# Optimization experiments

Measured on AMD Instinct MI355X. Metric: run time of the kernel, lower is better.

The kernel has to match this reference:

```python
import jax, jax.numpy as jnp
import numpy as np

N = 50000      # nodes
E = 800000     # edges (avg degree 16)
B = 8          # graphs in batch
H = 128        # hidden (message_passer out_channels)
FF = 64        # fourier_feat_dim -> fourier features have dim 2*FF
REPEATS = 4    # repeats_training
OUT = 4        # output_dim
IN_X = 5
IN_MASK = 3

def _fourier(x, M):
    # https://arxiv.org/pdf/2106.02795.pdf : [cos(xM), sin(xM)] / sqrt(2F)
    p = x @ M
    return jnp.concatenate([jnp.cos(p), jnp.sin(p)], axis=-1) / jnp.sqrt(2.0 * M.shape[1])

def _seg_mean(v, idx, n):
    s = jax.ops.segment_sum(v, idx, num_segments=n)
    c = jax.ops.segment_sum(jnp.ones((v.shape[0],), v.dtype), idx, num_segments=n)
    return s / jnp.maximum(c, 1.0)[:, None]

def setup_inputs() -> dict:
    key = jax.random.key(0)
    ks = jax.random.split(key, 16)
    x = jax.random.normal(ks[0], (N, IN_X), jnp.float32)
    x_mask = jax.random.bernoulli(ks[1], 0.1, (N, IN_MASK)).astype(jnp.float32)
    edge_index = jax.random.randint(ks[2], (2, E), 0, N)
    edge_attr = jax.random.normal(ks[3], (E, 3), jnp.float32)
    pos = jax.random.uniform(ks[4], (N, 2), jnp.float32)
    batch = jnp.sort(jax.random.randint(ks[5], (N,), 0, B))
    sampling_points = jax.random.uniform(ks[6], (2,), jnp.float32)
    fourier_mat = jax.random.normal(ks[7], (2, FF), jnp.float32)  # learnable, init N(0,1)
    W_enc = jax.random.normal(ks[8], (IN_X + IN_MASK, H), jnp.float32) * 0.1
    b_enc = jnp.zeros((H,), jnp.float32)
    W_msg = jax.random.normal(ks[9], (2 * H + 3, H), jnp.float32) * 0.05
    b_msg = jnp.zeros((H,), jnp.float32)
    W_upd = jax.random.normal(ks[10], (4 * H, H), jnp.float32) * 0.05
    b_upd = jnp.zeros((H,), jnp.float32)
    W_dec = jax.random.normal(ks[11], (H, OUT), jnp.float32) * 0.1
    b_dec = jnp.zeros((OUT,), jnp.float32)
    return dict(x=x, x_mask=x_mask, edge_index=edge_index, edge_attr=edge_attr,
                pos=pos, batch=batch, sampling_points=sampling_points,
                fourier_mat=fourier_mat, W_enc=W_enc, b_enc=b_enc,
                W_msg=W_msg, b_msg=b_msg, W_upd=W_upd, b_upd=b_upd,
                W_dec=W_dec, b_dec=b_dec)

def reference(x, x_mask, edge_index, edge_attr, pos, batch, sampling_points,
              fourier_mat, W_enc, b_enc, W_msg, b_msg, W_upd, b_upd, W_dec, b_dec):
    bc = x_mask[:, -1]                                   # 0/1 BC flag
    x_full = jnp.concatenate([x, x_mask], axis=1)        # x = concat([x, x_mask])
    keys_ff = _fourier(pos, fourier_mat)                 # input fourier features [N, 2F]
    h = jax.nn.relu(x_full @ W_enc + b_enc)              # encoder -> [N, H]

    # x_BC: scatter-mean over BC nodes per graph (computed once)
    bc_sum = jax.ops.segment_sum(h * bc[:, None], batch, num_segments=B)
    bc_cnt = jax.ops.segment_sum(bc, batch, num_segments=B)
    x_BC = bc_sum / jnp.maximum(bc_cnt, 1.0)[:, None]    # [B, H]

    x_graph = _seg_mean(h, batch, B)                     # global_mean_pool [B, H]
    src, dst = edge_index[0], edge_index[1]
    deg = jnp.maximum(jax.ops.segment_sum(jnp.ones((E,), h.dtype), dst, num_segments=N), 1.0)

    for _ in range(REPEATS):  # repeated message passing
        m = jax.nn.relu(jnp.concatenate([h[src], h[dst], edge_attr], axis=1) @ W_msg + b_msg)
        agg = jax.ops.segment_sum(m, dst, num_segments=N) / deg[:, None]  # scatter-mean
        upd_in = jnp.concatenate([h, agg, x_graph[batch], x_BC[batch]], axis=1)
        h = h + jax.nn.relu(upd_in @ W_upd + b_upd)
        x_graph = _seg_mean(h, batch, B)                 # re-pool each repeat

    decoded = h @ W_dec + b_dec                          # [N, OUT]

    # kernelized fourier-feature interpolation at the sampling point
    q = _fourier(sampling_points, fourier_mat)           # [2F]
    nq = q / jnp.linalg.norm(q)
    nk = keys_ff / jnp.linalg.norm(keys_ff, axis=1, keepdims=True)
    vals_sum = h.sum(axis=0)                             # [H]
    kwv = nk.T @ h                                       # [2F, H]
    ks_sum = nk.sum(axis=0)                              # [2F]
    enc = (vals_sum + nq @ kwv) / (N + nq @ ks_sum)      # [H]
    U_sampled = enc @ W_dec + b_dec                      # [OUT]
    # pack (U_sampled, decoded) into one array: row 0 = sampled point, rows 1: = nodes
    return jnp.concatenate([U_sampled[None, :], decoded], axis=0)
```

## Files before the change

kernel.cpp:

```cpp
#include <hip/hip_runtime.h>
#include <math.h>

#define Nn 50000
#define Ee 800000
#define Bb 8
#define ROUNDS 4
#define KWVB 512
#define SCB 196
#define AP 40
#define HP 132
#define KS 40
#define NBK 196
#define P1B 391
#define CHUNK 2047

typedef __attribute__((ext_vector_type(8))) short bf16x8;
typedef __attribute__((ext_vector_type(4))) float f32x4;

__device__ inline short f2bf(float f) {
  union { float f; unsigned u; } v; v.f = f;
  unsigned r = v.u + 0x7fff + ((v.u >> 16) & 1);
  return (short)(r >> 16);
}
__device__ inline float bf2f(short s) {
  union { float f; unsigned u; } v; v.u = ((unsigned)(unsigned short)s) << 16;
  return v.f;
}

__global__ __launch_bounds__(256) void encode_seg(
    const float* __restrict__ x, const float* __restrict__ xm,
    const int* __restrict__ batch, const float* __restrict__ W,
    const float* __restrict__ b, float* __restrict__ h,
    float* __restrict__ gsum, float* __restrict__ gcnt,
    float* __restrict__ bcsum, float* __restrict__ bccnt) {
  __shared__ float xs5[128 * 5];
  __shared__ float xm3[128 * 3];
  __shared__ float ls[Bb * 128];
  __shared__ float lb[Bb * 128];
  __shared__ float lc[Bb], lbc[Bb];
  const int t = threadIdx.x;
  const int nBase = blockIdx.x * 128;
  const int j = t & 127, half = t >> 7;
  const int base5 = nBase * 5, base3 = nBase * 3;
  for (int q = t; q < 640; q += 256) xs5[q] = (base5 + q < Nn * 5) ? x[base5 + q] : 0.f;
  for (int q = t; q < 384; q += 256) xm3[q] = (base3 + q < Nn * 3) ? xm[base3 + q] : 0.f;
  for (int q = t; q < Bb * 128; q += 256) { ls[q] = 0.f; lb[q] = 0.f; }
  if (t < Bb) { lc[t] = 0.f; lbc[t] = 0.f; }
  float Wcol[8];
#pragma unroll
  for (int k = 0; k < 8; k++) Wcol[k] = W[k * 128 + j];
  const float bj = b[j];
  __syncthreads();
  int curb = -1;
  float runh = 0.f, runb = 0.f, runc = 0.f, runbc = 0.f;
  for (int kk = 0; kk < 64; kk++) {
    int i = nBase + kk * 2 + half;
    if (i >= Nn) break;
    int li = i - nBase;
    float acc = bj;
#pragma unroll
    for (int k = 0; k < 5; k++) acc = fmaf(xs5[li * 5 + k], Wcol[k], acc);
#pragma unroll
    for (int k = 0; k < 3; k++) acc = fmaf(xm3[li * 3 + k], Wcol[5 + k], acc);
    float v = fmaxf(acc, 0.f);
    h[(size_t)i * 128 + j] = v;
    float bc = xm3[li * 3 + 2];
    int g = batch[i];
    if (g != curb) {
      if (curb >= 0) {
        atomicAdd(&ls[curb * 128 + j], runh);
        atomicAdd(&lb[curb * 128 + j], runb);
        if (j == 0) { atomicAdd(&lc[curb], runc); atomicAdd(&lbc[curb], runbc); }
      }
      curb = g; runh = runb = runc = runbc = 0.f;
    }
    runh += v; runb += v * bc;
    if (j == 0) { runc += 1.f; runbc += bc; }
  }
  if (curb >= 0) {
    atomicAdd(&ls[curb * 128 + j], runh);
    atomicAdd(&lb[curb * 128 + j], runb);
    if (j == 0) { atomicAdd(&lc[curb], runc); atomicAdd(&lbc[curb], runbc); }
  }
  __syncthreads();
  for (int q = t; q < Bb * 128; q += 256) {
    float a = ls[q], c = lb[q];
    if (a != 0.f) atomicAdd(&gsum[q], a);
    if (c != 0.f) atomicAdd(&bcsum[q], c);
  }
  if (t < Bb) { atomicAdd(&gcnt[t], lc[t]); atomicAdd(&bccnt[t], lbc[t]); }
}

__global__ __launch_bounds__(256) void split_w_kernel(
    const float* __restrict__ Wm, const float* __restrict__ Wu,
    short* __restrict__ Wmt_h, short* __restrict__ Wmt_l,
    short* __restrict__ Wut_h, short* __restrict__ Wut_l) {
  int idx = blockIdx.x * 256 + threadIdx.x;
  if (idx < 32768) {
    int k = idx & 127, n = (idx >> 7) & 127, y = idx >> 14;
    float w = Wm[(size_t)(y * 128 + k) * 128 + n];
    short hi = f2bf(w);
    Wmt_h[idx] = hi;
    Wmt_l[idx] = f2bf(w - bf2f(hi));
  } else if (idx < 65536) {
    int j = idx - 32768;
    int k = j & 255, n = j >> 8;
    float w = Wu[(size_t)k * 128 + n];
    short hi = f2bf(w);
    Wut_h[j] = hi;
    Wut_l[j] = f2bf(w - bf2f(hi));
  }
}

__global__ __launch_bounds__(256) void bkt_cnt(const int* __restrict__ ei,
                                               int* __restrict__ bktcnt) {
  __shared__ int hist[NBK];
  int t = threadIdx.x;
  for (int q = t; q < NBK; q += 256) hist[q] = 0;
  __syncthreads();
  int base = blockIdx.x * CHUNK;
  int end = base + CHUNK < Ee ? base + CHUNK : Ee;
  for (int e = base + t; e < end; e += 256) atomicAdd(&hist[ei[Ee + e] >> 8], 1);
  __syncthreads();
  for (int q = t; q < NBK; q += 256)
    if (hist[q]) atomicAdd(&bktcnt[q], hist[q]);
}
__global__ __launch_bounds__(256) void bkt_scan(const int* __restrict__ bktcnt,
                                                int* __restrict__ bktbase,
                                                int* __restrict__ bktcur) {
  __shared__ int s[256];
  int t = threadIdx.x;
  int v = (t < NBK) ? bktcnt[t] : 0;
  s[t] = v;
  __syncthreads();
  for (int off = 1; off < 256; off <<= 1) {
    int x = (t >= off) ? s[t - off] : 0;
    __syncthreads();
    s[t] += x;
    __syncthreads();
  }
  int ex = s[t] - v;
  if (t < NBK) { bktbase[t] = ex; bktcur[t] = ex; }
  if (t == NBK - 1) bktbase[NBK] = ex + v;
}
__global__ __launch_bounds__(256) void bkt_part(
    const int* __restrict__ ei, const float* __restrict__ ea,
    int* __restrict__ bktcur, int2* __restrict__ recA,
    unsigned char* __restrict__ dlo) {
  __shared__ int hist[NBK], lbase[NBK], lcur[NBK];
  int t = threadIdx.x;
  for (int q = t; q < NBK; q += 256) hist[q] = 0;
  __syncthreads();
  int base = blockIdx.x * CHUNK;
  int end = base + CHUNK < Ee ? base + CHUNK : Ee;
  for (int e = base + t; e < end; e += 256) atomicAdd(&hist[ei[Ee + e] >> 8], 1);
  __syncthreads();
  for (int q = t; q < NBK; q += 256) {
    int c = hist[q];
    lbase[q] = c ? atomicAdd(&bktcur[q], c) : 0;
    lcur[q] = 0;
  }
  __syncthreads();
  for (int e = base + t; e < end; e += 256) {
    int d = ei[Ee + e];
    int bk = d >> 8;
    int p = lbase[bk] + atomicAdd(&lcur[bk], 1);
    unsigned r0 = (unsigned)ei[e] |
                  ((unsigned)(unsigned short)f2bf(ea[3 * (size_t)e + 0]) << 16);
    unsigned r1 = (unsigned)(unsigned short)f2bf(ea[3 * (size_t)e + 1]) |
                  ((unsigned)(unsigned short)f2bf(ea[3 * (size_t)e + 2]) << 16);
    recA[p] = make_int2((int)r0, (int)r1);
    dlo[p] = (unsigned char)(d & 255);
  }
}
__global__ __launch_bounds__(256) void dst_cnt(const int* __restrict__ bktbase,
                                               const unsigned char* __restrict__ dlo,
                                               int* __restrict__ cnt) {
  __shared__ int hh[256];
  int t = threadIdx.x;
  hh[t] = 0;
  __syncthreads();
  int b = blockIdx.x;
  int lo = bktbase[b], hi = bktbase[b + 1];
  for (int i = lo + t; i < hi; i += 256) atomicAdd(&hh[dlo[i]], 1);
  __syncthreads();
  int d = b * 256 + t;
  if (d < Nn) cnt[d] = hh[t];
}
__global__ __launch_bounds__(256) void bsum_kernel(const int* __restrict__ cnt,
                                                   int* __restrict__ bsum) {
  __shared__ int wsum[4];
  int t = threadIdx.x;
  int i = blockIdx.x * 256 + t;
  int v = (i < Nn) ? cnt[i] : 0;
#pragma unroll
  for (int off = 32; off > 0; off >>= 1) v += __shfl_down(v, off);
  if ((t & 63) == 0) wsum[t >> 6] = v;
  __syncthreads();
  if (t == 0) bsum[blockIdx.x] = wsum[0] + wsum[1] + wsum[2] + wsum[3];
}
__global__ __launch_bounds__(256) void scan_top_kernel(const int* __restrict__ bsum,
                                                       int* __restrict__ boff) {
  __shared__ int s[256];
  int t = threadIdx.x;
  int v = (t < SCB) ? bsum[t] : 0;
  s[t] = v;
  __syncthreads();
  for (int off = 1; off < 256; off <<= 1) {
    int x = (t >= off) ? s[t - off] : 0;
    __syncthreads();
    s[t] += x;
    __syncthreads();
  }
  boff[t] = s[t] - v;
}
__global__ __launch_bounds__(256) void apply_kernel(
    const int* __restrict__ cnt, const int* __restrict__ boff,
    int* __restrict__ rowptr, float* __restrict__ invdeg) {
  __shared__ int s[256];
  int t = threadIdx.x;
  int i = blockIdx.x * 256 + t;
  int v = (i < Nn) ? cnt[i] : 0;
  s[t] = v;
  __syncthreads();
  for (int off = 1; off < 256; off <<= 1) {
    int x = (t >= off) ? s[t - off] : 0;
    __syncthreads();
    s[t] += x;
    __syncthreads();
  }
  int ex = boff[blockIdx.x] + s[t] - v;
  if (i < Nn) {
    rowptr[i] = ex;
    invdeg[i] = 1.0f / fmaxf((float)v, 1.0f);
    if (i == Nn - 1) rowptr[Nn] = ex + v;
  }
}
__global__ __launch_bounds__(256) void bkt_fin(
    const int* __restrict__ bktbase, const int2* __restrict__ recA,
    const unsigned char* __restrict__ dlo, const int* __restrict__ rowptr,
    int2* __restrict__ rec) {
  __shared__ int cur[256];
  int t = threadIdx.x;
  int b = blockIdx.x;
  int d = b * 256 + t;
  cur[t] = (d < Nn) ? rowptr[d] : 0;
  __syncthreads();
  int lo = bktbase[b], hi = bktbase[b + 1];
  for (int i = lo + t; i < hi; i += 256) {
    int dl = dlo[i];
    int p = atomicAdd(&cur[dl], 1);
    rec[p] = recA[i];
  }
}

__global__ __launch_bounds__(128) void gb_static_kernel(
    const float* __restrict__ bcsum, const float* __restrict__ bccnt,
    const float* __restrict__ Wu, const float* __restrict__ bu,
    float* __restrict__ gbst) {
  __shared__ float xb[128];
  int g = blockIdx.x, t = threadIdx.x;
  xb[t] = bcsum[g * 128 + t] / fmaxf(bccnt[g], 1.f);
  __syncthreads();
  float acc = bu[t];
#pragma unroll 4
  for (int k = 0; k < 128; k++) acc = fmaf(xb[k], Wu[(size_t)(384 + k) * 128 + t], acc);
  gbst[g * 128 + t] = acc;
}

__global__ __launch_bounds__(128) void gb_dyn_kernel(
    const float* __restrict__ gsum, const float* __restrict__ gcnt,
    const float* __restrict__ gbst, const float* __restrict__ Wu,
    float* __restrict__ gb) {
  __shared__ float xg[128];
  int g = blockIdx.x, t = threadIdx.x;
  xg[t] = gsum[g * 128 + t] / fmaxf(gcnt[g], 1.f);
  __syncthreads();
  float acc = gbst[g * 128 + t];
#pragma unroll 4
  for (int k = 0; k < 128; k++) acc = fmaf(xg[k], Wu[(size_t)(256 + k) * 128 + t], acc);
  gb[g * 128 + t] = acc;
}

__global__ __launch_bounds__(256) void proj_mfma(
    const float* __restrict__ h, const short* __restrict__ Wth,
    unsigned char* __restrict__ hs8, unsigned short* __restrict__ hdbf) {
  __shared__ short Ah_s[128 * AP];
  __shared__ short Bh_s[128 * AP];
  const int t = threadIdx.x;
  const int nBase = blockIdx.x * 128;
  const int yoff = blockIdx.y * 16384;
  const int wave = t >> 6, lane = t & 63;
  const int ml = lane & 15, quad = lane >> 4;
  const int ko = quad * 8;

  f32x4 acc[2][8];
#pragma unroll
  for (int nt = 0; nt < 2; nt++)
#pragma unroll
    for (int mt = 0; mt < 8; mt++)
#pragma unroll
      for (int q = 0; q < 4; q++) acc[nt][mt][q] = 0.f;

  const int srow = t >> 1;
  const int kc = (t & 1) * 16;
  const int nd0 = nBase + srow;
  const int nn = nd0 < Nn ? nd0 : Nn - 1;

  for (int c = 0; c < 4; c++) {
    const float* p = &h[(size_t)nn * 128 + c * 32 + kc];
    float4 u0 = *(const float4*)(p + 0);
    float4 u1 = *(const float4*)(p + 4);
    float4 u2 = *(const float4*)(p + 8);
    float4 u3 = *(const float4*)(p + 12);
    const int k0 = c * 32;
    const bf16x8 gb0 = *(const bf16x8*)&Wth[(size_t)yoff + srow * 128 + k0 + kc];
    const bf16x8 gb1 = *(const bf16x8*)&Wth[(size_t)yoff + srow * 128 + k0 + kc + 8];
    float xs[16] = {u0.x,u0.y,u0.z,u0.w, u1.x,u1.y,u1.z,u1.w,
                    u2.x,u2.y,u2.z,u2.w, u3.x,u3.y,u3.z,u3.w};
    bf16x8 vh0, vh1;
#pragma unroll
    for (int j = 0; j < 8; j++) vh0[j] = f2bf(xs[j]);
#pragma unroll
    for (int j = 0; j < 8; j++) vh1[j] = f2bf(xs[8 + j]);
    __syncthreads();
    *(bf16x8*)&Ah_s[srow * AP + kc] = vh0;
    *(bf16x8*)&Ah_s[srow * AP + kc + 8] = vh1;
    *(bf16x8*)&Bh_s[srow * AP + kc] = gb0;
    *(bf16x8*)&Bh_s[srow * AP + kc + 8] = gb1;
    __syncthreads();
#pragma unroll
    for (int mt = 0; mt < 8; mt++) {
      const int ar = (mt * 16 + ml) * AP + ko;
      bf16x8 ah = *(const bf16x8*)&Ah_s[ar];
#pragma unroll
      for (int nt = 0; nt < 2; nt++) {
        const int br = (wave * 32 + nt * 16 + ml) * AP + ko;
        bf16x8 bh = *(const bf16x8*)&Bh_s[br];
        acc[nt][mt] = __builtin_amdgcn_mfma_f32_16x16x32_bf16(ah, bh, acc[nt][mt], 0, 0, 0);
      }
    }
  }
  if (blockIdx.y == 0) {
#pragma unroll
    for (int nt = 0; nt < 2; nt++) {
      const int ch = wave * 32 + nt * 16 + ml;
#pragma unroll
      for (int mt = 0; mt < 8; mt++) {
#pragma unroll
        for (int q = 0; q < 4; q++) {
          int nd = nBase + mt * 16 + quad * 4 + q;
          if (nd < Nn) {
            int pk = __builtin_amdgcn_cvt_pk_fp8_f32(acc[nt][mt][q], acc[nt][mt][q], 0, false);
            hs8[(size_t)nd * 128 + ch] = (unsigned char)(pk & 0xff);
          }
        }
      }
    }
  } else {
#pragma unroll
    for (int nt = 0; nt < 2; nt++) {
      const int ch = wave * 32 + nt * 16 + ml;
#pragma unroll
      for (int mt = 0; mt < 8; mt++) {
#pragma unroll
        for (int q = 0; q < 4; q++) {
          int nd = nBase + mt * 16 + quad * 4 + q;
          if (nd < Nn) hdbf[(size_t)nd * 128 + ch] = (unsigned short)f2bf(acc[nt][mt][q]);
        }
      }
    }
  }
}

__global__ __launch_bounds__(256) void agg_kernel(
    const unsigned char* __restrict__ hs8, const unsigned short* __restrict__ hdbf,
    unsigned short* __restrict__ aggbf, const int2* __restrict__ rec,
    const int* __restrict__ rowptr, const float* __restrict__ invdeg,
    const float* __restrict__ Wm, const float* __restrict__ bm) {
  int t = threadIdx.x;
  int hw = t >> 5, lane = t & 31;
  int v = blockIdx.x * 8 + hw;
  if (v >= Nn) return;
  int c0 = lane * 4;
  const float4 We0 = *(const float4*)&Wm[(size_t)256 * 128 + c0];
  const float4 We1 = *(const float4*)&Wm[(size_t)257 * 128 + c0];
  const float4 We2 = *(const float4*)&Wm[(size_t)258 * 128 + c0];
  const float4 b4  = *(const float4*)&bm[c0];
  const ushort4 hd4 = *(const ushort4*)&hdbf[(size_t)v * 128 + c0];
  const float bx = b4.x + bf2f((short)hd4.x), by = b4.y + bf2f((short)hd4.y),
              bz = b4.z + bf2f((short)hd4.z), bw = b4.w + bf2f((short)hd4.w);
  float ax = 0.f, ay = 0.f, az = 0.f, aw = 0.f;
  float ax2 = 0.f, ay2 = 0.f, az2 = 0.f, aw2 = 0.f;
  const int r0 = rowptr[v], r1 = rowptr[v + 1];
  int e = r0;
  for (; e + 2 <= r1; e += 2) {
    int2 q0 = rec[e], q1 = rec[e + 1];
    int s0 = q0.x & 0xffff, s1 = q1.x & 0xffff;
    unsigned hr0 = *(const unsigned*)&hs8[(size_t)s0 * 128 + c0];
    unsigned hr1 = *(const unsigned*)&hs8[(size_t)s1 * 128 + c0];
    float e00 = bf2f((short)(q0.x >> 16));
    float e01 = bf2f((short)(q0.y & 0xffff));
    float e02 = bf2f((short)(q0.y >> 16));
    float e10 = bf2f((short)(q1.x >> 16));
    float e11 = bf2f((short)(q1.y & 0xffff));
    float e12 = bf2f((short)(q1.y >> 16));
    float h0x = __builtin_amdgcn_cvt_f32_fp8(hr0, 0);
    float h0y = __builtin_amdgcn_cvt_f32_fp8(hr0, 1);
    float h0z = __builtin_amdgcn_cvt_f32_fp8(hr0, 2);
    float h0w = __builtin_amdgcn_cvt_f32_fp8(hr0, 3);
    float h1x = __builtin_amdgcn_cvt_f32_fp8(hr1, 0);
    float h1y = __builtin_amdgcn_cvt_f32_fp8(hr1, 1);
    float h1z = __builtin_amdgcn_cvt_f32_fp8(hr1, 2);
    float h1w = __builtin_amdgcn_cvt_f32_fp8(hr1, 3);
    ax += fmaxf(fmaf(e00, We0.x, fmaf(e01, We1.x, fmaf(e02, We2.x, h0x + bx))), 0.f);
    ay += fmaxf(fmaf(e00, We0.y, fmaf(e01, We1.y, fmaf(e02, We2.y, h0y + by))), 0.f);
    az += fmaxf(fmaf(e00, We0.z, fmaf(e01, We1.z, fmaf(e02, We2.z, h0z + bz))), 0.f);
    aw += fmaxf(fmaf(e00, We0.w, fmaf(e01, We1.w, fmaf(e02, We2.w, h0w + bw))), 0.f);
    ax2 += fmaxf(fmaf(e10, We0.x, fmaf(e11, We1.x, fmaf(e12, We2.x, h1x + bx))), 0.f);
    ay2 += fmaxf(fmaf(e10, We0.y, fmaf(e11, We1.y, fmaf(e12, We2.y, h1y + by))), 0.f);
    az2 += fmaxf(fmaf(e10, We0.z, fmaf(e11, We1.z, fmaf(e12, We2.z, h1z + bz))), 0.f);
    aw2 += fmaxf(fmaf(e10, We0.w, fmaf(e11, We1.w, fmaf(e12, We2.w, h1w + bw))), 0.f);
  }
  if (e < r1) {
    int2 q0 = rec[e];
    int s0 = q0.x & 0xffff;
    unsigned hr0 = *(const unsigned*)&hs8[(size_t)s0 * 128 + c0];
    float e00 = bf2f((short)(q0.x >> 16));
    float e01 = bf2f((short)(q0.y & 0xffff));
    float e02 = bf2f((short)(q0.y >> 16));
    float h0x = __builtin_amdgcn_cvt_f32_fp8(hr0, 0);
    float h0y = __builtin_amdgcn_cvt_f32_fp8(hr0, 1);
    float h0z = __builtin_amdgcn_cvt_f32_fp8(hr0, 2);
    float h0w = __builtin_amdgcn_cvt_f32_fp8(hr0, 3);
    ax += fmaxf(fmaf(e00, We0.x, fmaf(e01, We1.x, fmaf(e02, We2.x, h0x + bx))), 0.f);
    ay += fmaxf(fmaf(e00, We0.y, fmaf(e01, We1.y, fmaf(e02, We2.y, h0y + by))), 0.f);
    az += fmaxf(fmaf(e00, We0.z, fmaf(e01, We1.z, fmaf(e02, We2.z, h0z + bz))), 0.f);
    aw += fmaxf(fmaf(e00, We0.w, fmaf(e01, We1.w, fmaf(e02, We2.w, h0w + bw))), 0.f);
  }
  const float idg = invdeg[v];
  ushort4 o;
  o.x = (unsigned short)f2bf((ax + ax2) * idg);
  o.y = (unsigned short)f2bf((ay + ay2) * idg);
  o.z = (unsigned short)f2bf((az + az2) * idg);
  o.w = (unsigned short)f2bf((aw + aw2) * idg);
  *(ushort4*)&aggbf[(size_t)v * 128 + c0] = o;
}

__global__ __launch_bounds__(256) void updg_mfma(
    float* __restrict__ h, const unsigned short* __restrict__ aggbf,
    const int* __restrict__ batch,
    const short* __restrict__ Wth, const short* __restrict__ Wtl,
    const float* __restrict__ gb, float* __restrict__ gsum_out) {
  __shared__ short Ah_s[128 * AP], Al_s[128 * AP];
  __shared__ short Bh_s[128 * AP], Bl_s[128 * AP];
  __shared__ float gbs[Bb * 128];
  __shared__ float ls[Bb * 128];
  const int t = threadIdx.x;
  const int nBase = blockIdx.x * 128;
  *(float4*)&gbs[t * 4] = *(const float4*)&gb[t * 4];
#pragma unroll
  for (int q = 0; q < 4; q++) ls[t + q * 256] = 0.f;

  const int wave = t >> 6, lane = t & 63;
  const int ml = lane & 15, quad = lane >> 4;
  const int ko = quad * 8;

  f32x4 acc[2][8];
#pragma unroll
  for (int nt = 0; nt < 2; nt++)
#pragma unroll
    for (int mt = 0; mt < 8; mt++)
#pragma unroll
      for (int q = 0; q < 4; q++) acc[nt][mt][q] = 0.f;

  const int srow = t >> 1;
  const int kc = (t & 1) * 16;
  const int nd0 = nBase + srow;
  const int nn = nd0 < Nn ? nd0 : Nn - 1;

  for (int c = 0; c < 8; c++) {
    const int k0 = c * 32;
    bf16x8 vh0, vh1, vl0, vl1;
    if (c < 4) {
      const float* p = &h[(size_t)nn * 128 + c * 32 + kc];
      float4 u0 = *(const float4*)(p + 0);
      float4 u1 = *(const float4*)(p + 4);
      float4 u2 = *(const float4*)(p + 8);
      float4 u3 = *(const float4*)(p + 12);
      float xs[16] = {u0.x,u0.y,u0.z,u0.w, u1.x,u1.y,u1.z,u1.w,
                      u2.x,u2.y,u2.z,u2.w, u3.x,u3.y,u3.z,u3.w};
#pragma unroll
      for (int j = 0; j < 8; j++) {
        short hi = f2bf(xs[j]);
        vh0[j] = hi; vl0[j] = f2bf(xs[j] - bf2f(hi));
      }
#pragma unroll
      for (int j = 0; j < 8; j++) {
        short hi = f2bf(xs[8 + j]);
        vh1[j] = hi; vl1[j] = f2bf(xs[8 + j] - bf2f(hi));
      }
    } else {
      const unsigned short* pa = &aggbf[(size_t)nn * 128 + (c - 4) * 32 + kc];
      vh0 = *(const bf16x8*)(pa);
      vh1 = *(const bf16x8*)(pa + 8);
    }
    const bf16x8 gb0 = *(const bf16x8*)&Wth[(size_t)srow * 256 + k0 + kc];
    const bf16x8 gb1 = *(const bf16x8*)&Wth[(size_t)srow * 256 + k0 + kc + 8];
    const bf16x8 gl0 = *(const bf16x8*)&Wtl[(size_t)srow * 256 + k0 + kc];
    const bf16x8 gl1 = *(const bf16x8*)&Wtl[(size_t)srow * 256 + k0 + kc + 8];
    __syncthreads();
    *(bf16x8*)&Ah_s[srow * AP + kc] = vh0;
    *(bf16x8*)&Ah_s[srow * AP + kc + 8] = vh1;
    if (c < 4) {
      *(bf16x8*)&Al_s[srow * AP + kc] = vl0;
      *(bf16x8*)&Al_s[srow * AP + kc + 8] = vl1;
    }
    *(bf16x8*)&Bh_s[srow * AP + kc] = gb0;
    *(bf16x8*)&Bh_s[srow * AP + kc + 8] = gb1;
    *(bf16x8*)&Bl_s[srow * AP + kc] = gl0;
    *(bf16x8*)&Bl_s[srow * AP + kc + 8] = gl1;
    __syncthreads();
    if (c < 4) {
#pragma unroll
      for (int mt = 0; mt < 8; mt++) {
        const int ar = (mt * 16 + ml) * AP + ko;
        bf16x8 ah = *(const bf16x8*)&Ah_s[ar];
        bf16x8 al = *(const bf16x8*)&Al_s[ar];
#pragma unroll
        for (int nt = 0; nt < 2; nt++) {
          const int br = (wave * 32 + nt * 16 + ml) * AP + ko;
          bf16x8 bh = *(const bf16x8*)&Bh_s[br];
          bf16x8 bl = *(const bf16x8*)&Bl_s[br];
          acc[nt][mt] = __builtin_amdgcn_mfma_f32_16x16x32_bf16(ah, bh, acc[nt][mt], 0, 0, 0);
          acc[nt][mt] = __builtin_amdgcn_mfma_f32_16x16x32_bf16(ah, bl, acc[nt][mt], 0, 0, 0);
          acc[nt][mt] = __builtin_amdgcn_mfma_f32_16x16x32_bf16(al, bh, acc[nt][mt], 0, 0, 0);
        }
      }
    } else {
#pragma unroll
      for (int mt = 0; mt < 8; mt++) {
        const int ar = (mt * 16 + ml) * AP + ko;
        bf16x8 ah = *(const bf16x8*)&Ah_s[ar];
#pragma unroll
        for (int nt = 0; nt < 2; nt++) {
          const int br = (wave * 32 + nt * 16 + ml) * AP + ko;
          bf16x8 bh = *(const bf16x8*)&Bh_s[br];
          bf16x8 bl = *(const bf16x8*)&Bl_s[br];
          acc[nt][mt] = __builtin_amdgcn_mfma_f32_16x16x32_bf16(ah, bh, acc[nt][mt], 0, 0, 0);
          acc[nt][mt] = __builtin_amdgcn_mfma_f32_16x16x32_bf16(ah, bl, acc[nt][mt], 0, 0, 0);
        }
      }
    }
  }
#pragma unroll
  for (int nt = 0; nt < 2; nt++) {
    const int ch = wave * 32 + nt * 16 + ml;
#pragma unroll
    for (int mt = 0; mt < 8; mt++) {
      int rbase = nBase + mt * 16 + quad * 4;
      float runv = 0.f;
      int curb = -1;
#pragma unroll
      for (int q = 0; q < 4; q++) {
        int nd = rbase + q;
        if (nd < Nn) {
          int bi = batch[nd];
          float u = fmaxf(acc[nt][mt][q] + gbs[bi * 128 + ch], 0.f);
          float hn = h[(size_t)nd * 128 + ch] + u;
          h[(size_t)nd * 128 + ch] = hn;
          if (bi != curb) {
            if (curb >= 0) atomicAdd(&ls[curb * 128 + ch], runv);
            curb = bi;
            runv = 0.f;
          }
          runv += hn;
        }
      }
      if (curb >= 0) atomicAdd(&ls[curb * 128 + ch], runv);
    }
  }
  __syncthreads();
#pragma unroll
  for (int q = 0; q < 4; q++) {
    int idx = t + q * 256;
    float v = ls[idx];
    if (v != 0.f) atomicAdd(&gsum_out[idx], v);
  }
}

__global__ __launch_bounds__(256) void kwv_kernel(
    const float* __restrict__ h, const float* __restrict__ pos,
    const float* __restrict__ Fm, const float* __restrict__ Wd,
    const float* __restrict__ bd, float* __restrict__ partial,
    float* __restrict__ ksum, float* __restrict__ out) {
  __shared__ float h_s[32 * HP];
  __shared__ short nkT[128 * KS];
  __shared__ short hT[128 * KS];
  __shared__ float wd[512];
  __shared__ float ksum_s[128];
  __shared__ float dsum[256];
  const int t = threadIdx.x;
  const int hr = t >> 3;
  const int hc = (t & 7) * 16;
  const int fg = (t & 7) * 8;
  const int wave = t >> 6, lane = t & 63;
  const int ml = lane & 15, quad = lane >> 4;
  const int ko = quad * 8;
  if (t < 128) { *(float4*)&wd[t * 4] = *(const float4*)&Wd[t * 4]; ksum_s[t] = 0.f; }
  const float bdv = bd[t & 3];
  const int dn = (t & 127) >> 2, dno = t & 3;
  const int dk0 = (t >> 7) * 64;
  f32x4 acc[2][8];
#pragma unroll
  for (int nt = 0; nt < 2; nt++)
#pragma unroll
    for (int mt = 0; mt < 8; mt++)
#pragma unroll
      for (int q = 0; q < 4; q++) acc[nt][mt][q] = 0.f;
  float klc[8], kls[8];
#pragma unroll
  for (int f = 0; f < 8; f++) { klc[f] = 0.f; kls[f] = 0.f; }

  int ptile = -1;
  const int nTiles = (Nn + 31) / 32;
  for (int tile = blockIdx.x; tile < nTiles; tile += gridDim.x) {
    const int gh = tile * 32 + hr;
    float4 hv0 = {0.f, 0.f, 0.f, 0.f}, hv1 = hv0, hv2 = hv0, hv3 = hv0;
    float cbuf[8], sbuf[8];
    if (gh < Nn) {
      const float* hp = &h[(size_t)gh * 128 + hc];
      hv0 = *(const float4*)(hp + 0);
      hv1 = *(const float4*)(hp + 4);
      hv2 = *(const float4*)(hp + 8);
      hv3 = *(const float4*)(hp + 12);
      const float px = pos[gh * 2 + 0], py = pos[gh * 2 + 1];
#pragma unroll
      for (int f = 0; f < 8; f++) {
        float p = px * Fm[fg + f] + py * Fm[64 + fg + f];
        cbuf[f] = cosf(p) * 0.125f;
        sbuf[f] = sinf(p) * 0.125f;
      }
    } else {
#pragma unroll
      for (int f = 0; f < 8; f++) { cbuf[f] = 0.f; sbuf[f] = 0.f; }
    }
    float xs[16] = {hv0.x,hv0.y,hv0.z,hv0.w, hv1.x,hv1.y,hv1.z,hv1.w,
                    hv2.x,hv2.y,hv2.z,hv2.w, hv3.x,hv3.y,hv3.z,hv3.w};
    __syncthreads();
    if (ptile >= 0 && t < 128) {
      int gn = ptile * 32 + dn;
      if (gn < Nn) out[4 + (size_t)gn * 4 + dno] = dsum[t] + dsum[t + 128] + bdv;
    }
    *(float4*)&h_s[hr * HP + hc + 0]  = hv0;
    *(float4*)&h_s[hr * HP + hc + 4]  = hv1;
    *(float4*)&h_s[hr * HP + hc + 8]  = hv2;
    *(float4*)&h_s[hr * HP + hc + 12] = hv3;
#pragma unroll
    for (int i = 0; i < 16; i++) hT[(hc + i) * KS + hr] = f2bf(xs[i]);
#pragma unroll
    for (int f = 0; f < 8; f++) {
      nkT[(fg + f) * KS + hr] = f2bf(cbuf[f]);
      nkT[(64 + fg + f) * KS + hr] = f2bf(sbuf[f]);
      klc[f] += cbuf[f];
      kls[f] += sbuf[f];
    }
    __syncthreads();
#pragma unroll
    for (int mt = 0; mt < 8; mt++) {
      bf16x8 ah = *(const bf16x8*)&nkT[(mt * 16 + ml) * KS + ko];
#pragma unroll
      for (int nt = 0; nt < 2; nt++) {
        bf16x8 bh = *(const bf16x8*)&hT[(wave * 32 + nt * 16 + ml) * KS + ko];
        acc[nt][mt] = __builtin_amdgcn_mfma_f32_16x16x32_bf16(ah, bh, acc[nt][mt], 0, 0, 0);
      }
    }
    {
      float s = 0.f;
#pragma unroll 4
      for (int kk = dk0; kk < dk0 + 64; kk++) {
        int k = (kk + dn) & 127;
        s = fmaf(h_s[dn * HP + k], wd[k * 4 + dno], s);
      }
      dsum[t] = s;
    }
    ptile = tile;
  }
  __syncthreads();
  if (ptile >= 0 && t < 128) {
    int gn = ptile * 32 + dn;
    if (gn < Nn) out[4 + (size_t)gn * 4 + dno] = dsum[t] + dsum[t + 128] + bdv;
  }
  float* pb = &partial[(size_t)blockIdx.x * 16384];
#pragma unroll
  for (int nt = 0; nt < 2; nt++) {
    const int col = wave * 32 + nt * 16 + ml;
#pragma unroll
    for (int mt = 0; mt < 8; mt++) {
#pragma unroll
      for (int q = 0; q < 4; q++) {
        int row = mt * 16 + quad * 4 + q;
        pb[row * 128 + col] = acc[nt][mt][q];
      }
    }
  }
#pragma unroll
  for (int f = 0; f < 8; f++) {
    atomicAdd(&ksum_s[fg + f], klc[f]);
    atomicAdd(&ksum_s[64 + fg + f], kls[f]);
  }
  __syncthreads();
  if (t < 128) atomicAdd(&ksum[t], ksum_s[t]);
}

__global__ __launch_bounds__(256) void kwv_reduce(const float* __restrict__ partial,
                                                  float* __restrict__ kwv) {
  int idx = blockIdx.x * 256 + threadIdx.x;
  float s = 0.f;
  for (int b = 0; b < KWVB; b++) s += partial[(size_t)b * 16384 + idx];
  kwv[idx] = s;
}

__global__ __launch_bounds__(128) void final_kernel(
    const float* __restrict__ sp, const float* __restrict__ Fm,
    const float* __restrict__ kwv, const float* __restrict__ vs,
    const float* __restrict__ ksum, const float* __restrict__ Wd,
    const float* __restrict__ bd, float* __restrict__ out) {
  __shared__ float nq_s[128];
  __shared__ float red[2];
  __shared__ float redU[8];
  int t = threadIdx.x;
  int jj = t & 63;
  float p = sp[0] * Fm[jj] + sp[1] * Fm[64 + jj];
  nq_s[t] = ((t < 64) ? cosf(p) : sinf(p)) * 0.125f;
  __syncthreads();
  float num = 0.f;
#pragma unroll
  for (int g = 0; g < Bb; g++) num += vs[g * 128 + t];
  for (int k = 0; k < 128; k++) num = fmaf(nq_s[k], kwv[k * 128 + t], num);
  float dp = nq_s[t] * ksum[t];
#pragma unroll
  for (int off = 32; off > 0; off >>= 1) dp += __shfl_down(dp, off);
  if ((t & 63) == 0) red[t >> 6] = dp;
  __syncthreads();
  float den = (float)Nn + red[0] + red[1];
  float e = num / den;
  float u[4];
#pragma unroll
  for (int o = 0; o < 4; o++) u[o] = e * Wd[t * 4 + o];
#pragma unroll
  for (int off = 32; off > 0; off >>= 1) {
#pragma unroll
    for (int o = 0; o < 4; o++) u[o] += __shfl_down(u[o], off);
  }
  if ((t & 63) == 0) {
#pragma unroll
    for (int o = 0; o < 4; o++) redU[(t >> 6) * 4 + o] = u[o];
  }
  __syncthreads();
  if (t < 4) out[t] = redU[t] + redU[4 + t] + bd[t];
}

extern "C" void kernel_launch(void* const* d_in, const int* in_sizes, int n_in,
                              void* d_out, int out_size, void* d_ws, size_t ws_size,
                              hipStream_t stream) {
  const float* x    = (const float*)d_in[0];
  const float* xm   = (const float*)d_in[1];
  const int*   ei   = (const int*)d_in[2];
  const float* ea   = (const float*)d_in[3];
  const float* pos  = (const float*)d_in[4];
  const int*   batch= (const int*)d_in[5];
  const float* sp   = (const float*)d_in[6];
  const float* Fm   = (const float*)d_in[7];
  const float* Wenc = (const float*)d_in[8];
  const float* benc = (const float*)d_in[9];
  const float* Wmsg = (const float*)d_in[10];
  const float* bmsg = (const float*)d_in[11];
  const float* Wupd = (const float*)d_in[12];
  const float* bupd = (const float*)d_in[13];
  const float* Wdec = (const float*)d_in[14];
  const float* bdec = (const float*)d_in[15];
  float* out = (float*)d_out;

  float* ws     = (float*)d_ws;
  float* h      = ws;
  float* agg    = h + (size_t)Nn * 128;
  float* aux    = agg + (size_t)Nn * 128;
  float* invdeg = aux + (size_t)Nn * 128;
  float* gsum   = invdeg + Nn;
  float* gcnt   = gsum + 1024;
  float* bcsum  = gcnt + 8;
  float* bccnt  = bcsum + 1024;
  float* gsumR  = bccnt + 8;
  float* vsum   = gsumR + 4096;
  float* ksum   = vsum + 128;
  float* gbst   = ksum + 128;
  float* gbuf   = gbst + 1024;
  float* kwv    = gbuf + 4096;
  int2*  rec    = (int2*)(kwv + 16384);
  int*   cnt    = (int*)(rec + Ee);
  int*   rowptr = cnt + Nn;
  int*   bsum   = rowptr + Nn + 1;
  int*   boff   = bsum + 256;
  int*   bktcnt = boff + 256;
  int*   bktbase= bktcnt + 196;
  int*   bktcur = bktbase + 197;
  short* wmt_h  = (short*)(bktcur + 196);
  short* wmt_l  = wmt_h + 32768;
  short* wut_h  = wmt_l + 32768;
  short* wut_l  = wut_h + 32768;
  int2*  recA   = (int2*)(wut_l + 32768);
  unsigned char* dlo = (unsigned char*)(recA + Ee);

  unsigned short* aggbf = (unsigned short*)agg;
  unsigned char*  hs8   = (unsigned char*)aux;
  unsigned short* hdbf  = (unsigned short*)(hs8 + (size_t)Nn * 128);

  hipMemsetAsync(gsum, 0, 6416 * sizeof(float), stream);
  hipMemsetAsync(bktcnt, 0, 196 * sizeof(int), stream);

  split_w_kernel<<<256, 256, 0, stream>>>(Wmsg, Wupd, wmt_h, wmt_l, wut_h, wut_l);

  bkt_cnt<<<P1B, 256, 0, stream>>>(ei, bktcnt);
  bkt_scan<<<1, 256, 0, stream>>>(bktcnt, bktbase, bktcur);
  bkt_part<<<P1B, 256, 0, stream>>>(ei, ea, bktcur, recA, dlo);
  dst_cnt<<<NBK, 256, 0, stream>>>(bktbase, dlo, cnt);
  bsum_kernel<<<SCB, 256, 0, stream>>>(cnt, bsum);
  scan_top_kernel<<<1, 256, 0, stream>>>(bsum, boff);
  apply_kernel<<<SCB, 256, 0, stream>>>(cnt, boff, rowptr, invdeg);
  bkt_fin<<<NBK, 256, 0, stream>>>(bktbase, recA, dlo, rowptr, rec);

  const int nb128 = (Nn + 127) / 128;
  encode_seg<<<nb128, 256, 0, stream>>>(x, xm, batch, Wenc, benc, h,
                                        gsum, gcnt, bcsum, bccnt);
  gb_static_kernel<<<Bb, 128, 0, stream>>>(bcsum, bccnt, Wupd, bupd, gbst);
  gb_dyn_kernel<<<Bb, 128, 0, stream>>>(gsum, gcnt, gbst, Wupd, gbuf);

  for (int r = 0; r < ROUNDS; r++) {
    proj_mfma<<<dim3(nb128, 2), 256, 0, stream>>>(h, wmt_h, hs8, hdbf);
    agg_kernel<<<(Nn + 7) / 8, 256, 0, stream>>>(hs8, hdbf, aggbf, rec, rowptr,
                                                 invdeg, Wmsg, bmsg);
    updg_mfma<<<nb128, 256, 0, stream>>>(h, aggbf, batch, wut_h, wut_l,
                                         gbuf + r * 1024, gsumR + r * 1024);
    if (r < ROUNDS - 1)
      gb_dyn_kernel<<<Bb, 128, 0, stream>>>(gsumR + r * 1024, gcnt, gbst, Wupd,
                                            gbuf + (r + 1) * 1024);
  }

  kwv_kernel<<<KWVB, 256, 0, stream>>>(h, pos, Fm, Wdec, bdec, agg, ksum, out);
  kwv_reduce<<<64, 256, 0, stream>>>(agg, kwv);
  final_kernel<<<1, 128, 0, stream>>>(sp, Fm, kwv, gsumR + 3 * 1024, ksum,
                                      Wdec, bdec, out);
}
```

Before: 675.5 us.

## Fuse projection into encode/update kernels and merge CSR-build and graph-bias launches

```diff
diff --git a/kernel.cpp b/kernel.cpp
--- a/kernel.cpp
+++ b/kernel.cpp
@@ -10,6 +10,7 @@
 #define AP 40
 #define HP 132
 #define KS 40
+#define HT 136
 #define NBK 196
 #define P1B 391
 #define CHUNK 2047
@@ -27,17 +28,80 @@
   return v.f;
 }
 
-__global__ __launch_bounds__(256) void encode_seg(
+__device__ __forceinline__ void proj_from_lds(
+    const short* hnT, const short* __restrict__ Wth,
+    unsigned char* __restrict__ hs8, unsigned short* __restrict__ hdbf,
+    int nBase, int t) {
+  const int wave = t >> 6, lane = t & 63;
+  const int ml = lane & 15, quad = lane >> 4;
+  const int ko = quad * 8;
+#pragma unroll 1
+  for (int y = 0; y < 2; y++) {
+    f32x4 acc[2][8];
+#pragma unroll
+    for (int nt = 0; nt < 2; nt++)
+#pragma unroll
+      for (int mt = 0; mt < 8; mt++)
+#pragma unroll
+        for (int q = 0; q < 4; q++) acc[nt][mt][q] = 0.f;
+#pragma unroll
+    for (int c = 0; c < 4; c++) {
+      const bf16x8 b0 = *(const bf16x8*)&Wth[(size_t)y * 16384 + (wave * 32 + ml) * 128 + c * 32 + ko];
+      const bf16x8 b1 = *(const bf16x8*)&Wth[(size_t)y * 16384 + (wave * 32 + 16 + ml) * 128 + c * 32 + ko];
+#pragma unroll
+      for (int mt = 0; mt < 8; mt++) {
+        bf16x8 ah = *(const bf16x8*)&hnT[(mt * 16 + ml) * HT + c * 32 + ko];
+        acc[0][mt] = __builtin_amdgcn_mfma_f32_16x16x32_bf16(ah, b0, acc[0][mt], 0, 0, 0);
+        acc[1][mt] = __builtin_amdgcn_mfma_f32_16x16x32_bf16(ah, b1, acc[1][mt], 0, 0, 0);
+      }
+    }
+    if (y == 0) {
+#pragma unroll
+      for (int nt = 0; nt < 2; nt++) {
+        const int ch = wave * 32 + nt * 16 + ml;
+#pragma unroll
+        for (int mt = 0; mt < 8; mt++) {
+#pragma unroll
+          for (int q = 0; q < 4; q++) {
+            int nd = nBase + mt * 16 + quad * 4 + q;
+            if (nd < Nn) {
+              int pk = __builtin_amdgcn_cvt_pk_fp8_f32(acc[nt][mt][q], acc[nt][mt][q], 0, false);
+              hs8[(size_t)nd * 128 + ch] = (unsigned char)(pk & 0xff);
+            }
+          }
+        }
+      }
+    } else {
+#pragma unroll
+      for (int nt = 0; nt < 2; nt++) {
+        const int ch = wave * 32 + nt * 16 + ml;
+#pragma unroll
+        for (int mt = 0; mt < 8; mt++) {
+#pragma unroll
+          for (int q = 0; q < 4; q++) {
+            int nd = nBase + mt * 16 + quad * 4 + q;
+            if (nd < Nn) hdbf[(size_t)nd * 128 + ch] = (unsigned short)f2bf(acc[nt][mt][q]);
+          }
+        }
+      }
+    }
+  }
+}
+
+__global__ __launch_bounds__(256) void encode_proj(
     const float* __restrict__ x, const float* __restrict__ xm,
     const int* __restrict__ batch, const float* __restrict__ W,
     const float* __restrict__ b, float* __restrict__ h,
     float* __restrict__ gsum, float* __restrict__ gcnt,
-    float* __restrict__ bcsum, float* __restrict__ bccnt) {
+    float* __restrict__ bcsum, float* __restrict__ bccnt,
+    const short* __restrict__ Wmth, unsigned char* __restrict__ hs8,
+    unsigned short* __restrict__ hdbf) {
   __shared__ float xs5[128 * 5];
   __shared__ float xm3[128 * 3];
   __shared__ float ls[Bb * 128];
   __shared__ float lb[Bb * 128];
   __shared__ float lc[Bb], lbc[Bb];
+  __shared__ short hnT[128 * HT];
   const int t = threadIdx.x;
   const int nBase = blockIdx.x * 128;
   const int j = t & 127, half = t >> 7;
@@ -46,6 +110,11 @@
   for (int q = t; q < 384; q += 256) xm3[q] = (base3 + q < Nn * 3) ? xm[base3 + q] : 0.f;
   for (int q = t; q < Bb * 128; q += 256) { ls[q] = 0.f; lb[q] = 0.f; }
   if (t < Bb) { lc[t] = 0.f; lbc[t] = 0.f; }
+  {
+    const int nrem = Nn - nBase;
+    if (nrem < 128)
+      for (int q = nrem * HT + t; q < 128 * HT; q += 256) hnT[q] = 0;
+  }
   float Wcol[8];
 #pragma unroll
   for (int k = 0; k < 8; k++) Wcol[k] = W[k * 128 + j];
@@ -64,6 +133,7 @@
     for (int k = 0; k < 3; k++) acc = fmaf(xm3[li * 3 + k], Wcol[5 + k], acc);
     float v = fmaxf(acc, 0.f);
     h[(size_t)i * 128 + j] = v;
+    hnT[li * HT + j] = f2bf(v);
     float bc = xm3[li * 3 + 2];
     int g = batch[i];
     if (g != curb) {
@@ -89,6 +159,7 @@
     if (c != 0.f) atomicAdd(&bcsum[q], c);
   }
   if (t < Bb) { atomicAdd(&gcnt[t], lc[t]); atomicAdd(&bccnt[t], lbc[t]); }
+  proj_from_lds(hnT, Wmth, hs8, hdbf, nBase, t);
 }
 
 __global__ __launch_bounds__(256) void split_w_kernel(
@@ -173,10 +244,11 @@
     dlo[p] = (unsigned char)(d & 255);
   }
 }
-__global__ __launch_bounds__(256) void dst_cnt(const int* __restrict__ bktbase,
-                                               const unsigned char* __restrict__ dlo,
-                                               int* __restrict__ cnt) {
+__global__ __launch_bounds__(256) void dst_cnt_bsum(
+    const int* __restrict__ bktbase, const unsigned char* __restrict__ dlo,
+    int* __restrict__ cnt, int* __restrict__ bsum) {
   __shared__ int hh[256];
+  __shared__ int wsum[4];
   int t = threadIdx.x;
   hh[t] = 0;
   __syncthreads();
@@ -185,19 +257,13 @@
   for (int i = lo + t; i < hi; i += 256) atomicAdd(&hh[dlo[i]], 1);
   __syncthreads();
   int d = b * 256 + t;
-  if (d < Nn) cnt[d] = hh[t];
-}
-__global__ __launch_bounds__(256) void bsum_kernel(const int* __restrict__ cnt,
-                                                   int* __restrict__ bsum) {
-  __shared__ int wsum[4];
-  int t = threadIdx.x;
-  int i = blockIdx.x * 256 + t;
-  int v = (i < Nn) ? cnt[i] : 0;
+  int v = hh[t];
+  if (d < Nn) cnt[d] = v;
 #pragma unroll
   for (int off = 32; off > 0; off >>= 1) v += __shfl_down(v, off);
   if ((t & 63) == 0) wsum[t >> 6] = v;
   __syncthreads();
-  if (t == 0) bsum[blockIdx.x] = wsum[0] + wsum[1] + wsum[2] + wsum[3];
+  if (t == 0) bsum[b] = wsum[0] + wsum[1] + wsum[2] + wsum[3];
 }
 __global__ __launch_bounds__(256) void scan_top_kernel(const int* __restrict__ bsum,
                                                        int* __restrict__ boff) {
@@ -214,12 +280,16 @@
   }
   boff[t] = s[t] - v;
 }
-__global__ __launch_bounds__(256) void apply_kernel(
+__global__ __launch_bounds__(256) void apply_fin(
     const int* __restrict__ cnt, const int* __restrict__ boff,
-    int* __restrict__ rowptr, float* __restrict__ invdeg) {
+    const int* __restrict__ bktbase, const int2* __restrict__ recA,
+    const unsigned char* __restrict__ dlo,
+    int* __restrict__ rowptr, float* __restrict__ invdeg,
+    int2* __restrict__ rec) {
   __shared__ int s[256];
-  int t = threadIdx.x;
-  int i = blockIdx.x * 256 + t;
+  __shared__ int cur[256];
+  int t = threadIdx.x, b = blockIdx.x;
+  int i = b * 256 + t;
   int v = (i < Nn) ? cnt[i] : 0;
   s[t] = v;
   __syncthreads();
@@ -229,28 +299,19 @@
     s[t] += x;
     __syncthreads();
   }
-  int ex = boff[blockIdx.x] + s[t] - v;
+  int ex = boff[b] + s[t] - v;
   if (i < Nn) {
     rowptr[i] = ex;
     invdeg[i] = 1.0f / fmaxf((float)v, 1.0f);
     if (i == Nn - 1) rowptr[Nn] = ex + v;
   }
-}
-__global__ __launch_bounds__(256) void bkt_fin(
-    const int* __restrict__ bktbase, const int2* __restrict__ recA,
-    const unsigned char* __restrict__ dlo, const int* __restrict__ rowptr,
-    int2* __restrict__ rec) {
-  __shared__ int cur[256];
-  int t = threadIdx.x;
-  int b = blockIdx.x;
-  int d = b * 256 + t;
-  cur[t] = (d < Nn) ? rowptr[d] : 0;
+  cur[t] = ex;
   __syncthreads();
   int lo = bktbase[b], hi = bktbase[b + 1];
-  for (int i = lo + t; i < hi; i += 256) {
-    int dl = dlo[i];
+  for (int ii = lo + t; ii < hi; ii += 256) {
+    int dl = dlo[ii];
     int p = atomicAdd(&cur[dl], 1);
-    rec[p] = recA[i];
+    rec[p] = recA[ii];
   }
 }
 
@@ -266,111 +327,6 @@
 #pragma unroll 4
   for (int k = 0; k < 128; k++) acc = fmaf(xb[k], Wu[(size_t)(384 + k) * 128 + t], acc);
   gbst[g * 128 + t] = acc;
-}
-
-__global__ __launch_bounds__(128) void gb_dyn_kernel(
-    const float* __restrict__ gsum, const float* __restrict__ gcnt,
-    const float* __restrict__ gbst, const float* __restrict__ Wu,
-    float* __restrict__ gb) {
-  __shared__ float xg[128];
-  int g = blockIdx.x, t = threadIdx.x;
-  xg[t] = gsum[g * 128 + t] / fmaxf(gcnt[g], 1.f);
-  __syncthreads();
-  float acc = gbst[g * 128 + t];
-#pragma unroll 4
-  for (int k = 0; k < 128; k++) acc = fmaf(xg[k], Wu[(size_t)(256 + k) * 128 + t], acc);
-  gb[g * 128 + t] = acc;
-}
-
-__global__ __launch_bounds__(256) void proj_mfma(
-    const float* __restrict__ h, const short* __restrict__ Wth,
-    unsigned char* __restrict__ hs8, unsigned short* __restrict__ hdbf) {
-  __shared__ short Ah_s[128 * AP];
-  __shared__ short Bh_s[128 * AP];
-  const int t = threadIdx.x;
-  const int nBase = blockIdx.x * 128;
-  const int yoff = blockIdx.y * 16384;
-  const int wave = t >> 6, lane = t & 63;
-  const int ml = lane & 15, quad = lane >> 4;
-  const int ko = quad * 8;
-
-  f32x4 acc[2][8];
-#pragma unroll
-  for (int nt = 0; nt < 2; nt++)
-#pragma unroll
-    for (int mt = 0; mt < 8; mt++)
-#pragma unroll
-      for (int q = 0; q < 4; q++) acc[nt][mt][q] = 0.f;
-
-  const int srow = t >> 1;
-  const int kc = (t & 1) * 16;
-  const int nd0 = nBase + srow;
-  const int nn = nd0 < Nn ? nd0 : Nn - 1;
-
-  for (int c = 0; c < 4; c++) {
-    const float* p = &h[(size_t)nn * 128 + c * 32 + kc];
-    float4 u0 = *(const float4*)(p + 0);
-    float4 u1 = *(const float4*)(p + 4);
-    float4 u2 = *(const float4*)(p + 8);
-    float4 u3 = *(const float4*)(p + 12);
-    const int k0 = c * 32;
-    const bf16x8 gb0 = *(const bf16x8*)&Wth[(size_t)yoff + srow * 128 + k0 + kc];
-    const bf16x8 gb1 = *(const bf16x8*)&Wth[(size_t)yoff + srow * 128 + k0 + kc + 8];
-    float xs[16] = {u0.x,u0.y,u0.z,u0.w, u1.x,u1.y,u1.z,u1.w,
-                    u2.x,u2.y,u2.z,u2.w, u3.x,u3.y,u3.z,u3.w};
-    bf16x8 vh0, vh1;
-#pragma unroll
-    for (int j = 0; j < 8; j++) vh0[j] = f2bf(xs[j]);
-#pragma unroll
-    for (int j = 0; j < 8; j++) vh1[j] = f2bf(xs[8 + j]);
-    __syncthreads();
-    *(bf16x8*)&Ah_s[srow * AP + kc] = vh0;
-    *(bf16x8*)&Ah_s[srow * AP + kc + 8] = vh1;
-    *(bf16x8*)&Bh_s[srow * AP + kc] = gb0;
-    *(bf16x8*)&Bh_s[srow * AP + kc + 8] = gb1;
-    __syncthreads();
-#pragma unroll
-    for (int mt = 0; mt < 8; mt++) {
-      const int ar = (mt * 16 + ml) * AP + ko;
-      bf16x8 ah = *(const bf16x8*)&Ah_s[ar];
-#pragma unroll
-      for (int nt = 0; nt < 2; nt++) {
-        const int br = (wave * 32 + nt * 16 + ml) * AP + ko;
-        bf16x8 bh = *(const bf16x8*)&Bh_s[br];
-        acc[nt][mt] = __builtin_amdgcn_mfma_f32_16x16x32_bf16(ah, bh, acc[nt][mt], 0, 0, 0);
-      }
-    }
-  }
-  if (blockIdx.y == 0) {
-#pragma unroll
-    for (int nt = 0; nt < 2; nt++) {
-      const int ch = wave * 32 + nt * 16 + ml;
-#pragma unroll
-      for (int mt = 0; mt < 8; mt++) {
-#pragma unroll
-        for (int q = 0; q < 4; q++) {
-          int nd = nBase + mt * 16 + quad * 4 + q;
-          if (nd < Nn) {
-            int pk = __builtin_amdgcn_cvt_pk_fp8_f32(acc[nt][mt][q], acc[nt][mt][q], 0, false);
-            hs8[(size_t)nd * 128 + ch] = (unsigned char)(pk & 0xff);
-          }
-        }
-      }
-    }
-  } else {
-#pragma unroll
-    for (int nt = 0; nt < 2; nt++) {
-      const int ch = wave * 32 + nt * 16 + ml;
-#pragma unroll
-      for (int mt = 0; mt < 8; mt++) {
-#pragma unroll
-        for (int q = 0; q < 4; q++) {
-          int nd = nBase + mt * 16 + quad * 4 + q;
-          if (nd < Nn) hdbf[(size_t)nd * 128 + ch] = (unsigned short)f2bf(acc[nt][mt][q]);
-        }
-      }
-    }
-  }
 }
 
 __global__ __launch_bounds__(256) void agg_kernel(
@@ -447,24 +403,57 @@
   *(ushort4*)&aggbf[(size_t)v * 128 + c0] = o;
 }
 
-__global__ __launch_bounds__(256) void updg_mfma(
+__global__ __launch_bounds__(256) void updg_fused(
     float* __restrict__ h, const unsigned short* __restrict__ aggbf,
     const int* __restrict__ batch,
     const short* __restrict__ Wth, const short* __restrict__ Wtl,
-    const float* __restrict__ gb, float* __restrict__ gsum_out) {
-  __shared__ short Ah_s[128 * AP], Al_s[128 * AP];
-  __shared__ short Bh_s[128 * AP], Bl_s[128 * AP];
+    const float* __restrict__ Wu, const float* __restrict__ gbst,
+    const float* __restrict__ gsum_in, const float* __restrict__ gcnt,
+    float* __restrict__ gsum_out,
+    const short* __restrict__ Wmth, unsigned char* __restrict__ hs8,
+    unsigned short* __restrict__ hdbf, int doproj) {
+  __shared__ short ms[4 * 128 * AP];
   __shared__ float gbs[Bb * 128];
   __shared__ float ls[Bb * 128];
+  short* Ah_s = ms;
+  short* Al_s = ms + 128 * AP;
+  short* Bh_s = ms + 2 * 128 * AP;
+  short* Bl_s = ms + 3 * 128 * AP;
+  short* hnT  = ms;
+  float* xg   = (float*)ms;
+
   const int t = threadIdx.x;
   const int nBase = blockIdx.x * 128;
-  *(float4*)&gbs[t * 4] = *(const float4*)&gb[t * 4];
-#pragma unroll
-  for (int q = 0; q < 4; q++) ls[t + q * 256] = 0.f;
-
   const int wave = t >> 6, lane = t & 63;
   const int ml = lane & 15, quad = lane >> 4;
   const int ko = quad * 8;
+
+  {
+    int g4 = t >> 5;
+    float ic = 1.f / fmaxf(gcnt[g4], 1.f);
+    float4 gs = *(const float4*)&gsum_in[t * 4];
+    gs.x *= ic; gs.y *= ic; gs.z *= ic; gs.w *= ic;
+    *(float4*)&xg[t * 4] = gs;
+  }
+#pragma unroll
+  for (int q = 0; q < 4; q++) ls[t + q * 256] = 0.f;
+  __syncthreads();
+  {
+    const int ch = t & 127, g0 = (t >> 7) * 4;
+    float a0 = 0.f, a1 = 0.f, a2 = 0.f, a3 = 0.f;
+#pragma unroll 4
+    for (int k = 0; k < 128; k++) {
+      float w = Wu[(size_t)(256 + k) * 128 + ch];
+      a0 = fmaf(xg[(g0 + 0) * 128 + k], w, a0);
+      a1 = fmaf(xg[(g0 + 1) * 128 + k], w, a1);
+      a2 = fmaf(xg[(g0 + 2) * 128 + k], w, a2);
+      a3 = fmaf(xg[(g0 + 3) * 128 + k], w, a3);
+    }
+    gbs[(g0 + 0) * 128 + ch] = gbst[(g0 + 0) * 128 + ch] + a0;
+    gbs[(g0 + 1) * 128 + ch] = gbst[(g0 + 1) * 128 + ch] + a1;
+    gbs[(g0 + 2) * 128 + ch] = gbst[(g0 + 2) * 128 + ch] + a2;
+    gbs[(g0 + 3) * 128 + ch] = gbst[(g0 + 3) * 128 + ch] + a3;
+  }
 
   f32x4 acc[2][8];
 #pragma unroll
@@ -553,12 +542,15 @@
       }
     }
   }
+  __syncthreads();
+
 #pragma unroll
   for (int nt = 0; nt < 2; nt++) {
     const int ch = wave * 32 + nt * 16 + ml;
 #pragma unroll
     for (int mt = 0; mt < 8; mt++) {
-      int rbase = nBase + mt * 16 + quad * 4;
+      int lrb = mt * 16 + quad * 4;
+      int rbase = nBase + lrb;
       float runv = 0.f;
       int curb = -1;
 #pragma unroll
@@ -569,6 +561,7 @@
           float u = fmaxf(acc[nt][mt][q] + gbs[bi * 128 + ch], 0.f);
           float hn = h[(size_t)nd * 128 + ch] + u;
           h[(size_t)nd * 128 + ch] = hn;
+          hnT[(lrb + q) * HT + ch] = f2bf(hn);
           if (bi != curb) {
             if (curb >= 0) atomicAdd(&ls[curb * 128 + ch], runv);
             curb = bi;
@@ -587,6 +580,7 @@
     float v = ls[idx];
     if (v != 0.f) atomicAdd(&gsum_out[idx], v);
   }
+  if (doproj) proj_from_lds(hnT, Wmth, hs8, hdbf, nBase, t);
 }
 
 __global__ __launch_bounds__(256) void kwv_kernel(
@@ -824,27 +818,25 @@
   bkt_cnt<<<P1B, 256, 0, stream>>>(ei, bktcnt);
   bkt_scan<<<1, 256, 0, stream>>>(bktcnt, bktbase, bktcur);
   bkt_part<<<P1B, 256, 0, stream>>>(ei, ea, bktcur, recA, dlo);
-  dst_cnt<<<NBK, 256, 0, stream>>>(bktbase, dlo, cnt);
-  bsum_kernel<<<SCB, 256, 0, stream>>>(cnt, bsum);
+  dst_cnt_bsum<<<NBK, 256, 0, stream>>>(bktbase, dlo, cnt, bsum);
   scan_top_kernel<<<1, 256, 0, stream>>>(bsum, boff);
-  apply_kernel<<<SCB, 256, 0, stream>>>(cnt, boff, rowptr, invdeg);
-  bkt_fin<<<NBK, 256, 0, stream>>>(bktbase, recA, dlo, rowptr, rec);
+  apply_fin<<<NBK, 256, 0, stream>>>(cnt, boff, bktbase, recA, dlo,
+                                     rowptr, invdeg, rec);
 
   const int nb128 = (Nn + 127) / 128;
-  encode_seg<<<nb128, 256, 0, stream>>>(x, xm, batch, Wenc, benc, h,
-                                        gsum, gcnt, bcsum, bccnt);
+  encode_proj<<<nb128, 256, 0, stream>>>(x, xm, batch, Wenc, benc, h,
+                                         gsum, gcnt, bcsum, bccnt,
+                                         wmt_h, hs8, hdbf);
   gb_static_kernel<<<Bb, 128, 0, stream>>>(bcsum, bccnt, Wupd, bupd, gbst);
-  gb_dyn_kernel<<<Bb, 128, 0, stream>>>(gsum, gcnt, gbst, Wupd, gbuf);
 
   for (int r = 0; r < ROUNDS; r++) {
-    proj_mfma<<<dim3(nb128, 2), 256, 0, stream>>>(h, wmt_h, hs8, hdbf);
     agg_kernel<<<(Nn + 7) / 8, 256, 0, stream>>>(hs8, hdbf, aggbf, rec, rowptr,
                                                  invdeg, Wmsg, bmsg);
-    updg_mfma<<<nb128, 256, 0, stream>>>(h, aggbf, batch, wut_h, wut_l,
-                                         gbuf + r * 1024, gsumR + r * 1024);
-    if (r < ROUNDS - 1)
-      gb_dyn_kernel<<<Bb, 128, 0, stream>>>(gsumR + r * 1024, gcnt, gbst, Wupd,
-                                            gbuf + (r + 1) * 1024);
+    updg_fused<<<nb128, 256, 0, stream>>>(
+        h, aggbf, batch, wut_h, wut_l, Wupd, gbst,
+        (r == 0) ? gsum : (gsumR + (size_t)(r - 1) * 1024), gcnt,
+        gsumR + (size_t)r * 1024, wmt_h, hs8, hdbf,
+        (r < ROUNDS - 1) ? 1 : 0);
   }
 
   kwv_kernel<<<KWVB, 256, 0, stream>>>(h, pos, Fm, Wdec, bdec, agg, ksum, out);
```

Result: slower. 777.1 us (+15.0%).
